# Kernel optimization log

Hardware: AMD Instinct MI355X
Metric: run time of the kernel (lower is better)

The kernel has to match this reference:

```python
import jax, jax.numpy as jnp
import numpy as np

B, N, C, DK, TOPK = 4, 4096, 256, 64, 8


def setup_inputs() -> dict:
    key = jax.random.key(0)
    k1, k2, k3 = jax.random.split(key, 3)
    x = jax.random.normal(k1, (B, N, C), dtype=jnp.float32)
    # nn.Linear(channels, d_k, bias=False) weights, stored as [C, DK] for x @ W
    W_q = jax.random.normal(k2, (C, DK), dtype=jnp.float32) * (C ** -0.5)
    W_k = jax.random.normal(k3, (C, DK), dtype=jnp.float32) * (C ** -0.5)
    return {"x": x, "W_q": W_q, "W_k": W_k, "top_k": TOPK}


def reference(x, W_q, W_k, top_k):
    d_k = W_q.shape[-1]
    scale = d_k ** -0.5
    Q = x @ W_q                                   # [B, N, DK]
    K = x @ W_k                                   # [B, N, DK]
    S = jnp.einsum('bnd,bmd->bnm', Q, K) * scale  # [B, N, N]
    _, topk_idx = jax.lax.top_k(S, top_k)         # [B, N, top_k]
    n = S.shape[-1]
    # scatter True at top-k column indices per row (mirrors torch scatter_)
    row_mask = lambda idx: jnp.zeros((n,), dtype=bool).at[idx].set(True)
    mask = jax.vmap(jax.vmap(row_mask))(topk_idx)  # [B, N, N] bool
    S_masked = jnp.where(mask, S, -jnp.inf)
    A = jax.nn.softmax(S_masked, axis=-1)
    return A
```

## Files before the change

### kernel.cpp

```cpp
#include <hip/hip_runtime.h>
#include <math.h>

#define NROW 16384
#define NCOL 4096
#define CDIM 256
#define DKDIM 64
#define SCALE 0.125f

typedef float v4f __attribute__((ext_vector_type(4)));
typedef __attribute__((ext_vector_type(8))) short short8v;
typedef __attribute__((ext_vector_type(4))) float f32x4;

__device__ __forceinline__ unsigned mono(float v) {
  unsigned u = __float_as_uint(v);
  unsigned s = (unsigned)(((int)u) >> 31);
  return u ^ (s | 0x80000000u);
}
__device__ __forceinline__ float unmono(unsigned k) {
  unsigned u = (k & 0x80000000u) ? (k ^ 0x80000000u) : ~k;
  return __uint_as_float(u);
}
__device__ __forceinline__ unsigned short f2bf(float f) {
  unsigned u = __float_as_uint(f);
  u += 0x7FFFu + ((u >> 16) & 1u);
  return (unsigned short)(u >> 16);
}
__device__ __forceinline__ unsigned umaxu(unsigned a, unsigned b) { return a > b ? a : b; }

__device__ __forceinline__ void ins8(unsigned tk[8], unsigned& tmin, int& tmpos, unsigned v) {
  #pragma unroll
  for (int j = 0; j < 8; ++j) if (j == tmpos) tk[j] = v;
  tmin = tk[0]; tmpos = 0;
  #pragma unroll
  for (int j = 1; j < 8; ++j) if (tk[j] < tmin) { tmin = tk[j]; tmpos = j; }
}
__device__ __forceinline__ unsigned umax8(const unsigned kv[8]) {
  unsigned a = umaxu(umaxu(kv[0], kv[1]), umaxu(kv[2], kv[3]));
  unsigned b = umaxu(umaxu(kv[4], kv[5]), umaxu(kv[6], kv[7]));
  return umaxu(a, b);
}
__device__ __forceinline__ void seed8r(const unsigned kv[8],
                                       unsigned tk[8], unsigned& tmin, int& tmpos) {
  #pragma unroll
  for (int j = 0; j < 8; ++j) tk[j] = kv[j];
  tmin = tk[0]; tmpos = 0;
  #pragma unroll
  for (int j = 1; j < 8; ++j) if (tk[j] < tmin) { tmin = tk[j]; tmpos = j; }
}
__device__ __forceinline__ void scan8r(const unsigned kvin[8],
                                       unsigned tk[8], unsigned& tmin, int& tmpos) {
  unsigned kv[8];
  #pragma unroll
  for (int j = 0; j < 8; ++j) kv[j] = kvin[j];
  unsigned gm = umax8(kv);
  #pragma unroll
  for (int pass = 0; pass < 2; ++pass) {
    if (__any(gm > tmin)) {
      if (gm > tmin) {
        ins8(tk, tmin, tmpos, gm);
        #pragma unroll
        for (int j = 0; j < 8; ++j) if (kv[j] == gm) kv[j] = 0u;
      }
      gm = umax8(kv);
    }
  }
  if (__any(gm > tmin)) {
    #pragma unroll
    for (int j = 0; j < 8; ++j) if (kv[j] > tmin) ins8(tk, tmin, tmpos, kv[j]);
  }
}
__device__ __forceinline__ void seed8(const unsigned* __restrict__ sp,
                                      unsigned tk[8], unsigned& tmin, int& tmpos) {
  uint4 ka = *(const uint4*)(sp);
  uint4 kb = *(const uint4*)(sp + 4);
  unsigned kv[8] = {ka.x, ka.y, ka.z, ka.w, kb.x, kb.y, kb.z, kb.w};
  seed8r(kv, tk, tmin, tmpos);
}
__device__ __forceinline__ void scan8(const unsigned* __restrict__ sp,
                                      unsigned tk[8], unsigned& tmin, int& tmpos) {
  uint4 ka = *(const uint4*)(sp);
  uint4 kb = *(const uint4*)(sp + 4);
  unsigned kv[8] = {ka.x, ka.y, ka.z, ka.w, kb.x, kb.y, kb.z, kb.w};
  scan8r(kv, tk, tmin, tmpos);
}

__global__ __launch_bounds__(512, 2) void qk_proj(
    const float* __restrict__ x, const float* __restrict__ Wq,
    const float* __restrict__ Wk, float* __restrict__ Qt,
    float* __restrict__ Kt, unsigned short* __restrict__ Qh,
    unsigned short* __restrict__ Kh) {
  __shared__ float4 xs4[64][65];
  const int t = threadIdx.x;
  const int rb = blockIdx.x;
  {
    const float4* xg = (const float4*)(x + (size_t)rb * 64 * CDIM);
    #pragma unroll
    for (int i = 0; i < 8; ++i) {
      int idx = i * 512 + t;
      xs4[idx >> 6][idx & 63] = xg[idx];
    }
  }
  __syncthreads();

  const int lane = t & 63;
  const int wu = __builtin_amdgcn_readfirstlane(t >> 6);
  const int proj = wu >> 2;
  const int chunk = wu & 3;
  const float* __restrict__ Wp = proj ? Wk : Wq;

  float acc[16];
  #pragma unroll
  for (int j = 0; j < 16; ++j) acc[j] = 0.f;

  #pragma unroll 4
  for (int cs = 0; cs < 64; ++cs) {
    float4 xv = xs4[lane][cs];
    const float xc[4] = {xv.x, xv.y, xv.z, xv.w};
    #pragma unroll
    for (int i = 0; i < 4; ++i) {
      const float4* __restrict__ w4 =
          (const float4*)(Wp + (size_t)(cs * 4 + i) * DKDIM + chunk * 16);
      float4 wa = w4[0], wb = w4[1], wc = w4[2], wd = w4[3];
      float xi = xc[i];
      acc[0]  = fmaf(xi, wa.x, acc[0]);  acc[1]  = fmaf(xi, wa.y, acc[1]);
      acc[2]  = fmaf(xi, wa.z, acc[2]);  acc[3]  = fmaf(xi, wa.w, acc[3]);
      acc[4]  = fmaf(xi, wb.x, acc[4]);  acc[5]  = fmaf(xi, wb.y, acc[5]);
      acc[6]  = fmaf(xi, wb.z, acc[6]);  acc[7]  = fmaf(xi, wb.w, acc[7]);
      acc[8]  = fmaf(xi, wc.x, acc[8]);  acc[9]  = fmaf(xi, wc.y, acc[9]);
      acc[10] = fmaf(xi, wc.z, acc[10]); acc[11] = fmaf(xi, wc.w, acc[11]);
      acc[12] = fmaf(xi, wd.x, acc[12]); acc[13] = fmaf(xi, wd.y, acc[13]);
      acc[14] = fmaf(xi, wd.z, acc[14]); acc[15] = fmaf(xi, wd.w, acc[15]);
    }
  }

  const int gr = rb * 64 + lane;
  float* Of = (proj ? Kt : Qt) + (size_t)gr * 64 + chunk * 16;
  #pragma unroll
  for (int i = 0; i < 4; ++i) {
    float4 o = {acc[4 * i], acc[4 * i + 1], acc[4 * i + 2], acc[4 * i + 3]};
    ((float4*)Of)[i] = o;
  }
  unsigned short* Oh = (proj ? Kh : Qh) + (size_t)gr * 64 + chunk * 16;
  unsigned hp[8];
  #pragma unroll
  for (int i = 0; i < 8; ++i)
    hp[i] = (unsigned)f2bf(acc[2 * i]) | ((unsigned)f2bf(acc[2 * i + 1]) << 16);
  uint4 h0 = {hp[0], hp[1], hp[2], hp[3]};
  uint4 h1 = {hp[4], hp[5], hp[6], hp[7]};
  ((uint4*)Oh)[0] = h0;
  ((uint4*)Oh)[1] = h1;
}

__global__ __launch_bounds__(256, 2) void s_fused(
    const unsigned short* __restrict__ Qh, const unsigned short* __restrict__ Kh,
    const float* __restrict__ Qt, const float* __restrict__ Kt,
    float* __restrict__ out) {
  __shared__ unsigned keys[32 * 260];
  __shared__ unsigned cand[32][64];
  __shared__ float    pval[32][8];
  __shared__ int      pcol[32][8];

  const int t = threadIdx.x;
  const int lane = t & 63;
  const int wu = __builtin_amdgcn_readfirstlane(t >> 6);
  const int rg = wu >> 1;
  const int h = wu & 1;
  const int bid = blockIdx.x;
  const int orig = (bid & 7) * 64 + (bid >> 3);
  const int blockrow = orig * 32;
  const int b = blockrow >> 12;

  const int l15 = lane & 15, lk = lane >> 4;
  const int rowg = blockrow + rg * 16 + l15;
  const short8v a0 = *(const short8v*)(Qh + (size_t)rowg * 64 + lk * 8);
  const short8v a1 = *(const short8v*)(Qh + (size_t)rowg * 64 + lk * 8 + 32);

  const unsigned short* Kb = Kh + ((size_t)(b << 12)) * 64;

  unsigned tk[4][8]; unsigned tmin[4]; int tmpos[4];
  #pragma unroll 1
  for (int g = 0; g < 16; ++g) {
    unsigned kv[4][8];
    #pragma unroll
    for (int t8 = 0; t8 < 8; ++t8) {
      const int col = h * 2048 + (g * 8 + t8) * 16 + l15;
      const unsigned short* kp = Kb + (size_t)col * 64 + lk * 8;
      const short8v b0 = *(const short8v*)(kp);
      const short8v b1 = *(const short8v*)(kp + 32);
      f32x4 acc = {0.f, 0.f, 0.f, 0.f};
      acc = __builtin_amdgcn_mfma_f32_16x16x32_bf16(a0, b0, acc, 0, 0, 0);
      acc = __builtin_amdgcn_mfma_f32_16x16x32_bf16(a1, b1, acc, 0, 0, 0);
      #pragma unroll
      for (int i = 0; i < 4; ++i)
        kv[i][t8] = (mono(acc[i]) & 0xFFFFF000u) | (unsigned)col;
    }
    if (g == 0) {
      #pragma unroll
      for (int i = 0; i < 4; ++i) seed8r(kv[i], tk[i], tmin[i], tmpos[i]);
    } else {
      #pragma unroll
      for (int i = 0; i < 4; ++i) scan8r(kv[i], tk[i], tmin[i], tmpos[i]);
    }
  }
  #pragma unroll
  for (int i = 0; i < 4; ++i) {
    unsigned* kr = keys + (rg * 16 + lk * 4 + i) * 260 + h * 128 + l15 * 8;
    uint4 s0 = {tk[i][0], tk[i][1], tk[i][2], tk[i][3]};
    uint4 s1 = {tk[i][4], tk[i][5], tk[i][6], tk[i][7]};
    ((uint4*)kr)[0] = s0; ((uint4*)kr)[1] = s1;
  }
  __syncthreads();

  {
    const int row = t >> 3, q = t & 7;
    const unsigned* sp = keys + row * 260 + q * 32;
    unsigned mt[8]; unsigned mmin; int mmpos;
    seed8(sp, mt, mmin, mmpos);
    scan8(sp + 8, mt, mmin, mmpos);
    scan8(sp + 16, mt, mmin, mmpos);
    scan8(sp + 24, mt, mmin, mmpos);
    uint4 o0 = {mt[0], mt[1], mt[2], mt[3]};
    uint4 o1 = {mt[4], mt[5], mt[6], mt[7]};
    uint4* cp = (uint4*)(&cand[row][q * 8]);
    cp[0] = o0; cp[1] = o1;
  }
  __syncthreads();

  #pragma unroll 1
  for (int p = 0; p < 8; ++p) {
    const int rr = p * 4 + wu;
    const unsigned key = cand[rr][lane];
    const int col = (int)(key & 0xFFFu);
    const float4* Kp = (const float4*)(Kt + ((size_t)((b << 12) + col)) * 64);
    const float4* Qp = (const float4*)(Qt + (size_t)(blockrow + rr) * 64);
    float s = 0.f;
    #pragma unroll
    for (int g2 = 0; g2 < 16; ++g2) {
      float4 qf = Qp[g2];
      float4 kf = Kp[g2];
      s = fmaf(qf.x, kf.x, s);
      s = fmaf(qf.y, kf.y, s);
      s = fmaf(qf.z, kf.z, s);
      s = fmaf(qf.w, kf.w, s);
    }
    unsigned kx = mono(s);
    float vals[8]; int cols[8];
    #pragma unroll
    for (int it = 0; it < 8; ++it) {
      unsigned m = kx;
      #pragma unroll
      for (int d = 1; d < 64; d <<= 1) m = umaxu(m, (unsigned)__shfl_xor((int)m, d, 64));
      unsigned long long win = __ballot(kx == m);
      int wl = (int)__ffsll(win) - 1;
      cols[it] = __shfl(col, wl, 64);
      vals[it] = unmono(m);
      if (lane == wl) kx = 0u;
    }
    float vq[8]; float sum = 0.f;
    #pragma unroll
    for (int it = 0; it < 8; ++it) { vq[it] = __expf((vals[it] - vals[0]) * SCALE); sum += vq[it]; }
    float inv = 1.f / sum;
    if (lane < 8) {
      pval[rr][lane] = vq[lane] * inv;
      pcol[rr][lane] = cols[lane];
    }
  }
  __syncthreads();

  #pragma unroll 1
  for (int j = 0; j < 8; ++j) {
    const int sr = wu * 8 + j;
    float vq[8]; int cols[8];
    #pragma unroll
    for (int q2 = 0; q2 < 8; ++q2) { vq[q2] = pval[sr][q2]; cols[q2] = pcol[sr][q2]; }
    v4f* orow4 = (v4f*)(out + ((size_t)(blockrow + sr) << 12));
    #pragma unroll
    for (int i = 0; i < 16; ++i) {
      const int base = i * 256 + lane * 4;
      v4f z = {0.f, 0.f, 0.f, 0.f};
      #pragma unroll
      for (int q2 = 0; q2 < 8; ++q2) {
        z.x = (cols[q2] == base)     ? vq[q2] : z.x;
        z.y = (cols[q2] == base + 1) ? vq[q2] : z.y;
        z.z = (cols[q2] == base + 2) ? vq[q2] : z.z;
        z.w = (cols[q2] == base + 3) ? vq[q2] : z.w;
      }
      __builtin_nontemporal_store(z, &orow4[(size_t)i * 64 + lane]);
    }
  }
}

extern "C" void kernel_launch(void* const* d_in, const int* in_sizes, int n_in,
                              void* d_out, int out_size, void* d_ws, size_t ws_size,
                              hipStream_t stream) {
  const float* x  = (const float*)d_in[0];
  const float* Wq = (const float*)d_in[1];
  const float* Wk = (const float*)d_in[2];
  float* out = (float*)d_out;

  char* ws = (char*)d_ws;
  float* Qt = (float*)ws;
  float* Kt = (float*)(ws + ((size_t)4 << 20));
  unsigned short* Qh = (unsigned short*)(ws + ((size_t)8 << 20));
  unsigned short* Kh = (unsigned short*)(ws + ((size_t)10 << 20));

  qk_proj<<<dim3(NROW / 64), 512, 0, stream>>>(x, Wq, Wk, Qt, Kt, Qh, Kh);
  s_fused<<<512, 256, 0, stream>>>(Qh, Kh, Qt, Kt, out);
}
```

Baseline: 448.6 us.

## Halve rows per block, split columns across four waves, zero-fill then scatter top-k

Each block now handles 16 rows instead of 32, and its four waves each scan a quarter of the 4096 columns. This doubles the grid to 1024 blocks and raises the occupancy hint to 4 blocks per CU. The candidate key buffer gets an XOR swizzle to avoid LDS bank conflicts, and the per-row probability arrays now alias that buffer to save shared memory. The output pass writes plain zeros with nontemporal stores, waits on vmcnt, then scatters the 8 softmax values. This removes the per-element compare/select work, but correctness depends on the zero store landing before the scatter store to the same address.

```diff
diff --git a/kernel.cpp b/kernel.cpp
--- a/kernel.cpp
+++ b/kernel.cpp
@@ -69,19 +69,16 @@
     for (int j = 0; j < 8; ++j) if (kv[j] > tmin) ins8(tk, tmin, tmpos, kv[j]);
   }
 }
-__device__ __forceinline__ void seed8(const unsigned* __restrict__ sp,
-                                      unsigned tk[8], unsigned& tmin, int& tmpos) {
-  uint4 ka = *(const uint4*)(sp);
-  uint4 kb = *(const uint4*)(sp + 4);
-  unsigned kv[8] = {ka.x, ka.y, ka.z, ka.w, kb.x, kb.y, kb.z, kb.w};
-  seed8r(kv, tk, tmin, tmpos);
-}
-__device__ __forceinline__ void scan8(const unsigned* __restrict__ sp,
-                                      unsigned tk[8], unsigned& tmin, int& tmpos) {
-  uint4 ka = *(const uint4*)(sp);
-  uint4 kb = *(const uint4*)(sp + 4);
-  unsigned kv[8] = {ka.x, ka.y, ka.z, ka.w, kb.x, kb.y, kb.z, kb.w};
-  scan8r(kv, tk, tmin, tmpos);
+
+__device__ __forceinline__ int kswz(int row, int off) {
+  return row * 512 + (off ^ (((off >> 6) & 7) << 2));
+}
+__device__ __forceinline__ void ld8swz(const unsigned* k, int row, int off,
+                                       unsigned kv[8]) {
+  uint4 ka = *(const uint4*)&k[kswz(row, off)];
+  uint4 kb = *(const uint4*)&k[kswz(row, off + 4)];
+  kv[0] = ka.x; kv[1] = ka.y; kv[2] = ka.z; kv[3] = ka.w;
+  kv[4] = kb.x; kv[5] = kb.y; kv[6] = kb.z; kv[7] = kb.w;
 }
 
 __global__ __launch_bounds__(512, 2) void qk_proj(
@@ -151,39 +148,36 @@
   ((uint4*)Oh)[1] = h1;
 }
 
-__global__ __launch_bounds__(256, 2) void s_fused(
+__global__ __launch_bounds__(256, 4) void s_fused(
     const unsigned short* __restrict__ Qh, const unsigned short* __restrict__ Kh,
     const float* __restrict__ Qt, const float* __restrict__ Kt,
     float* __restrict__ out) {
-  __shared__ unsigned keys[32 * 260];
-  __shared__ unsigned cand[32][64];
-  __shared__ float    pval[32][8];
-  __shared__ int      pcol[32][8];
+  __shared__ unsigned keys[16 * 512];
+  __shared__ unsigned cand[16][64];
+  float (*pval)[8] = (float(*)[8])keys;
+  int   (*pcol)[8] = (int(*)[8])(keys + 128);
 
   const int t = threadIdx.x;
   const int lane = t & 63;
   const int wu = __builtin_amdgcn_readfirstlane(t >> 6);
-  const int rg = wu >> 1;
-  const int h = wu & 1;
   const int bid = blockIdx.x;
-  const int orig = (bid & 7) * 64 + (bid >> 3);
-  const int blockrow = orig * 32;
+  const int orig = (bid & 7) * 128 + (bid >> 3);
+  const int blockrow = orig * 16;
   const int b = blockrow >> 12;
 
   const int l15 = lane & 15, lk = lane >> 4;
-  const int rowg = blockrow + rg * 16 + l15;
+  const int rowg = blockrow + l15;
   const short8v a0 = *(const short8v*)(Qh + (size_t)rowg * 64 + lk * 8);
   const short8v a1 = *(const short8v*)(Qh + (size_t)rowg * 64 + lk * 8 + 32);
-
   const unsigned short* Kb = Kh + ((size_t)(b << 12)) * 64;
 
   unsigned tk[4][8]; unsigned tmin[4]; int tmpos[4];
   #pragma unroll 1
-  for (int g = 0; g < 16; ++g) {
+  for (int g = 0; g < 8; ++g) {
     unsigned kv[4][8];
     #pragma unroll
     for (int t8 = 0; t8 < 8; ++t8) {
-      const int col = h * 2048 + (g * 8 + t8) * 16 + l15;
+      const int col = wu * 1024 + (g * 8 + t8) * 16 + l15;
       const unsigned short* kp = Kb + (size_t)col * 64 + lk * 8;
       const short8v b0 = *(const short8v*)(kp);
       const short8v b1 = *(const short8v*)(kp + 32);
@@ -204,30 +198,35 @@
   }
   #pragma unroll
   for (int i = 0; i < 4; ++i) {
-    unsigned* kr = keys + (rg * 16 + lk * 4 + i) * 260 + h * 128 + l15 * 8;
+    const int row = lk * 4 + i;
+    const int off = wu * 128 + l15 * 8;
     uint4 s0 = {tk[i][0], tk[i][1], tk[i][2], tk[i][3]};
     uint4 s1 = {tk[i][4], tk[i][5], tk[i][6], tk[i][7]};
-    ((uint4*)kr)[0] = s0; ((uint4*)kr)[1] = s1;
+    *(uint4*)&keys[kswz(row, off)] = s0;
+    *(uint4*)&keys[kswz(row, off + 4)] = s1;
   }
   __syncthreads();
 
-  {
-    const int row = t >> 3, q = t & 7;
-    const unsigned* sp = keys + row * 260 + q * 32;
-    unsigned mt[8]; unsigned mmin; int mmpos;
-    seed8(sp, mt, mmin, mmpos);
-    scan8(sp + 8, mt, mmin, mmpos);
-    scan8(sp + 16, mt, mmin, mmpos);
-    scan8(sp + 24, mt, mmin, mmpos);
+  if ((t & 15) < 8) {
+    const int row = t >> 4, s = t & 7;
+    const int base = s * 64;
+    unsigned kv[8]; unsigned mt[8]; unsigned mmin; int mmpos;
+    ld8swz(keys, row, base, kv);
+    seed8r(kv, mt, mmin, mmpos);
+    #pragma unroll
+    for (int m = 1; m < 8; ++m) {
+      ld8swz(keys, row, base + m * 8, kv);
+      scan8r(kv, mt, mmin, mmpos);
+    }
     uint4 o0 = {mt[0], mt[1], mt[2], mt[3]};
     uint4 o1 = {mt[4], mt[5], mt[6], mt[7]};
-    uint4* cp = (uint4*)(&cand[row][q * 8]);
+    uint4* cp = (uint4*)(&cand[row][s * 8]);
     cp[0] = o0; cp[1] = o1;
   }
   __syncthreads();
 
   #pragma unroll 1
-  for (int p = 0; p < 8; ++p) {
+  for (int p = 0; p < 4; ++p) {
     const int rr = p * 4 + wu;
     const unsigned key = cand[rr][lane];
     const int col = (int)(key & 0xFFFu);
@@ -267,26 +266,22 @@
   }
   __syncthreads();
 
-  #pragma unroll 1
-  for (int j = 0; j < 8; ++j) {
-    const int sr = wu * 8 + j;
-    float vq[8]; int cols[8];
-    #pragma unroll
-    for (int q2 = 0; q2 < 8; ++q2) { vq[q2] = pval[sr][q2]; cols[q2] = pcol[sr][q2]; }
-    v4f* orow4 = (v4f*)(out + ((size_t)(blockrow + sr) << 12));
-    #pragma unroll
-    for (int i = 0; i < 16; ++i) {
-      const int base = i * 256 + lane * 4;
-      v4f z = {0.f, 0.f, 0.f, 0.f};
-      #pragma unroll
-      for (int q2 = 0; q2 < 8; ++q2) {
-        z.x = (cols[q2] == base)     ? vq[q2] : z.x;
-        z.y = (cols[q2] == base + 1) ? vq[q2] : z.y;
-        z.z = (cols[q2] == base + 2) ? vq[q2] : z.z;
-        z.w = (cols[q2] == base + 3) ? vq[q2] : z.w;
-      }
-      __builtin_nontemporal_store(z, &orow4[(size_t)i * 64 + lane]);
-    }
+  {
+    const v4f z = {0.f, 0.f, 0.f, 0.f};
+    #pragma unroll 1
+    for (int j = 0; j < 4; ++j) {
+      const int sr = wu * 4 + j;
+      v4f* orow4 = (v4f*)(out + ((size_t)(blockrow + sr) << 12));
+      #pragma unroll
+      for (int i = 0; i < 16; ++i)
+        __builtin_nontemporal_store(z, &orow4[(size_t)i * 64 + lane]);
+    }
+  }
+  asm volatile("s_waitcnt vmcnt(0)" ::: "memory");
+  if (lane < 32) {
+    const int sr = wu * 4 + (lane >> 3);
+    const int q = lane & 7;
+    out[((size_t)(blockrow + sr) << 12) + (size_t)pcol[sr][q]] = pval[sr][q];
   }
 }
 
@@ -305,5 +300,5 @@
   unsigned short* Kh = (unsigned short*)(ws + ((size_t)10 << 20));
 
   qk_proj<<<dim3(NROW / 64), 512, 0, stream>>>(x, Wq, Wk, Qt, Kt, Qh, Kh);
-  s_fused<<<512, 256, 0, stream>>>(Qh, Kh, Qt, Kt, out);
-}
+  s_fused<<<1024, 256, 0, stream>>>(Qh, Kh, Qt, Kt, out);
+}
```

New measurement: 459.7 us. 2.5% more time.
